# Kernel optimization log

Measured on AMD Instinct MI355X. Metric: run time of the kernel, lower is better.

The kernel has to match this reference:

```python
import jax, jax.numpy as jnp
import numpy as np

N, V, I, O, G = 16, 4096, 128, 128, 16


def setup_inputs() -> dict:
    key = jax.random.key(0)
    ks = jax.random.split(key, 7)
    stdv = 1.0 / np.sqrt(O)  # reset_parameters: uniform(-stdv, stdv)
    u = lambda k, shape: jax.random.uniform(k, shape, jnp.float32, -stdv, stdv)
    return {
        "x": jax.random.normal(ks[0], (N, V, I), jnp.float32),
        "hx": jax.random.normal(ks[1], (N, V, O), jnp.float32),
        "group_index": jax.random.randint(ks[2], (V,), 0, G),
        "weight_ih": u(ks[3], (3, G, O, I)),
        "bias_ih": u(ks[4], (3, G, O)),
        "weight_hh": u(ks[5], (3, G, O, O)),
        "bias_hh": u(ks[6], (3, G, O)),
    }


def reference(x, hx, group_index, weight_ih, bias_ih, weight_hh, bias_hh):
    # gather per-node weights: [3, V, O, I] / [3, V, O]
    w_ih = weight_ih[:, group_index]
    b_ih = bias_ih[:, group_index]
    w_hh = weight_hh[:, group_index]
    b_hh = bias_hh[:, group_index]

    def lin_x(xx, w, b):  # [N,V,I] x [V,O,I] -> [N,V,O]
        return jnp.einsum("nvi,voi->nvo", xx, w) + b[None]

    def lin_h(h, w, b):  # torch einsum 'NVO,VOO->NVO' takes diagonal of w
        wd = jnp.diagonal(w, axis1=-2, axis2=-1)  # [V,O]
        return h * wd[None] + b[None]

    r = jax.nn.sigmoid(lin_x(x, w_ih[0], b_ih[0]) + lin_h(hx, w_hh[0], b_hh[0]))
    z = jax.nn.sigmoid(lin_x(x, w_ih[1], b_ih[1]) + lin_h(hx, w_hh[1], b_hh[1]))
    n = jnp.tanh(lin_x(x, w_ih[2], b_ih[2]) + r * lin_h(hx, w_hh[2], b_hh[2]))
    return (1.0 - z) * n + z * hx
```

## Files before the change

kernel.cpp:

```cpp
#include <hip/hip_runtime.h>
#include <math.h>

#define NN 16
#define VV 4096
#define II 128
#define OO 128
#define GG 16

typedef __attribute__((ext_vector_type(8))) short bf16x8;
typedef __attribute__((ext_vector_type(4))) float f32x4;

__device__ inline unsigned short f2bf(float f) {
    union { float f; unsigned u; } c; c.f = f;
    unsigned r = c.u + 0x7FFFu + ((c.u >> 16) & 1u);
    return (unsigned short)(r >> 16);
}
__device__ inline float bf2f(unsigned short h) {
    union { unsigned u; float f; } c; c.u = ((unsigned)h) << 16;
    return c.f;
}
__device__ inline void split1(float f, unsigned short& hi, unsigned short& lo) {
    hi = f2bf(f);
    lo = f2bf(f - bf2f(hi));
}
__device__ inline bf16x8 as_bf(uint4 u) {
    union { uint4 u; bf16x8 b; } c; c.u = u; return c.b;
}
__device__ inline void pack8(const float4& a, const float4& b, uint4& ph, uint4& pl) {
    unsigned short hi[8], lo[8];
    split1(a.x, hi[0], lo[0]); split1(a.y, hi[1], lo[1]);
    split1(a.z, hi[2], lo[2]); split1(a.w, hi[3], lo[3]);
    split1(b.x, hi[4], lo[4]); split1(b.y, hi[5], lo[5]);
    split1(b.z, hi[6], lo[6]); split1(b.w, hi[7], lo[7]);
    ph.x = (unsigned)hi[0] | ((unsigned)hi[1] << 16);
    ph.y = (unsigned)hi[2] | ((unsigned)hi[3] << 16);
    ph.z = (unsigned)hi[4] | ((unsigned)hi[5] << 16);
    ph.w = (unsigned)hi[6] | ((unsigned)hi[7] << 16);
    pl.x = (unsigned)lo[0] | ((unsigned)lo[1] << 16);
    pl.y = (unsigned)lo[2] | ((unsigned)lo[3] << 16);
    pl.z = (unsigned)lo[4] | ((unsigned)lo[5] << 16);
    pl.w = (unsigned)lo[6] | ((unsigned)lo[7] << 16);
}

__global__ __launch_bounds__(256) void prepack_kernel(
    const float* __restrict__ w_ih, uint4* __restrict__ wp)
{
    const int t  = blockIdx.x * 256 + threadIdx.x;
    const int i8 = t & 15;
    const int o  = (t >> 4) & 127;
    const int gg = t >> 11;

    const float* src = w_ih + ((size_t)gg * OO + o) * II + i8 * 8;
    const float4 a = *(const float4*)src;
    const float4 b = *(const float4*)(src + 4);
    uint4 ph, pl;
    pack8(a, b, ph, pl);

    const int s    = i8 >> 2;
    const int kb   = i8 & 3;
    const int lane = kb * 16 + (o & 15);
    const int ct   = o >> 4;
    const int pidx = ((gg * 8 + ct) * 4 + s) * 64 + lane;
    wp[pidx * 2]     = ph;
    wp[pidx * 2 + 1] = pl;
}

template <bool PREPACKED>
__global__ __launch_bounds__(256, 4) void ggru_mfma_kernel(
    const float* __restrict__ x,
    const float* __restrict__ hx,
    const int*   __restrict__ gidx,
    const uint4* __restrict__ wp,
    const float* __restrict__ w_ih,
    const float* __restrict__ b_ih,
    const float* __restrict__ w_hh,
    const float* __restrict__ b_hh,
    float*       __restrict__ out)
{
    const int v    = blockIdx.x;
    const int tid  = threadIdx.x;
    const int lane = tid & 63;
    const int wv   = tid >> 6;
    const int g    = gidx[v];

    __shared__ uint4 xhS[256];
    __shared__ uint4 xlS[256];
    __shared__ float gbuf[3][NN][132];

    {
        const int row = tid >> 4;
        const int sk  = tid & 15;
        const int s   = sk >> 2, kb = sk & 3;
        const float* xp = x + ((size_t)row * VV + v) * II + s * 32 + kb * 8;
        const float4 xa = *(const float4*)xp;
        const float4 xb = *(const float4*)(xp + 4);
        uint4 ph, pl;
        pack8(xa, xb, ph, pl);
        xhS[s * 64 + kb * 16 + row] = ph;
        xlS[s * 64 + kb * 16 + row] = pl;
    }
    __syncthreads();

    int tb[6];
    const float* wraw[6];
    #pragma unroll
    for (int t = 0; t < 6; ++t) {
        const int col  = wv * 96 + t * 16;
        const int gate = col >> 7;
        const int ob   = col & 127;
        const int ct   = ob >> 4;
        tb[t] = ((gate * GG + g) * 8 + ct) * 4;
        wraw[t] = w_ih + (((size_t)gate * GG + g) * OO + ob + (lane & 15)) * II + (lane >> 4) * 8;
    }

    f32x4 acc[6];
    #pragma unroll
    for (int t = 0; t < 6; ++t) acc[t] = (f32x4){0.f, 0.f, 0.f, 0.f};

    #pragma unroll
    for (int s = 0; s < 4; ++s) {
        const bf16x8 ah = as_bf(xhS[s * 64 + lane]);
        const bf16x8 al = as_bf(xlS[s * 64 + lane]);
        #pragma unroll
        for (int t = 0; t < 6; ++t) {
            bf16x8 wh, wl;
            if (PREPACKED) {
                wh = as_bf(wp[(size_t)(tb[t] + s) * 128 + lane * 2]);
                wl = as_bf(wp[(size_t)(tb[t] + s) * 128 + lane * 2 + 1]);
            } else {
                const float4 wa = *(const float4*)(wraw[t] + s * 32);
                const float4 wb = *(const float4*)(wraw[t] + s * 32 + 4);
                uint4 ph, pl;
                pack8(wa, wb, ph, pl);
                wh = as_bf(ph);
                wl = as_bf(pl);
            }
            acc[t] = __builtin_amdgcn_mfma_f32_16x16x32_bf16(ah, wh, acc[t], 0, 0, 0);
            acc[t] = __builtin_amdgcn_mfma_f32_16x16x32_bf16(al, wh, acc[t], 0, 0, 0);
            acc[t] = __builtin_amdgcn_mfma_f32_16x16x32_bf16(ah, wl, acc[t], 0, 0, 0);
        }
    }

    #pragma unroll
    for (int t = 0; t < 6; ++t) {
        const int col  = wv * 96 + t * 16 + (lane & 15);
        const int gate = col >> 7;
        const int o    = col & 127;
        #pragma unroll
        for (int r = 0; r < 4; ++r) {
            gbuf[gate][(lane >> 4) * 4 + r][o] = acc[t][r];
        }
    }
    __syncthreads();

    {
        const int o  = tid & 127;
        const int rb = (tid >> 7) * 8;

        const float bi0 = b_ih[(0 * GG + g) * OO + o];
        const float bi1 = b_ih[(1 * GG + g) * OO + o];
        const float bi2 = b_ih[(2 * GG + g) * OO + o];
        const float bh0 = b_hh[(0 * GG + g) * OO + o];
        const float bh1 = b_hh[(1 * GG + g) * OO + o];
        const float bh2 = b_hh[(2 * GG + g) * OO + o];
        const float wd0 = w_hh[((size_t)(0 * GG + g) * OO + o) * OO + o];
        const float wd1 = w_hh[((size_t)(1 * GG + g) * OO + o) * OO + o];
        const float wd2 = w_hh[((size_t)(2 * GG + g) * OO + o) * OO + o];

        #pragma unroll
        for (int r = 0; r < 8; ++r) {
            const int row = rb + r;
            const size_t idx = ((size_t)row * VV + v) * OO + o;
            const float h = hx[idx];

            const float gr  = gbuf[0][row][o] + bi0 + fmaf(h, wd0, bh0);
            const float gz  = gbuf[1][row][o] + bi1 + fmaf(h, wd1, bh1);
            const float ghn = fmaf(h, wd2, bh2);

            const float rr = 1.f / (1.f + __expf(-gr));
            const float zz = 1.f / (1.f + __expf(-gz));

            float t = gbuf[2][row][o] + bi2 + rr * ghn;
            t = fminf(fmaxf(t, -15.f), 15.f);
            const float e2 = __expf(2.f * t);
            const float th = (e2 - 1.f) / (e2 + 1.f);

            out[idx] = (1.f - zz) * th + zz * h;
        }
    }
}

extern "C" void kernel_launch(void* const* d_in, const int* in_sizes, int n_in,
                              void* d_out, int out_size, void* d_ws, size_t ws_size,
                              hipStream_t stream) {
    const float* x    = (const float*)d_in[0];
    const float* hx   = (const float*)d_in[1];
    const int*   gidx = (const int*)d_in[2];
    const float* w_ih = (const float*)d_in[3];
    const float* b_ih = (const float*)d_in[4];
    const float* w_hh = (const float*)d_in[5];
    const float* b_hh = (const float*)d_in[6];
    float* out = (float*)d_out;
    uint4* wp  = (uint4*)d_ws;

    const size_t need = 98304ull * 32ull;
    if (ws_size >= need) {
        prepack_kernel<<<384, 256, 0, stream>>>(w_ih, wp);
        ggru_mfma_kernel<true><<<VV, 256, 0, stream>>>(
            x, hx, gidx, wp, w_ih, b_ih, w_hh, b_hh, out);
    } else {
        ggru_mfma_kernel<false><<<VV, 256, 0, stream>>>(
            x, hx, gidx, (const uint4*)nullptr, w_ih, b_ih, w_hh, b_hh, out);
    }
}
```

Measured before the change: 176.9 us.

## Assign all three gates per output column to one wave, skip LDS gate buffer

Each wave now computes the r, z and n gate accumulators for the same 32 output columns, so the GRU epilogue reads its inputs straight from MFMA accumulator registers. This removes the shared-memory gate buffer, its scattered stores and the second block barrier, and it shrinks the LDS footprint. Weight fragments for a k-step are now all loaded before the MFMAs that use them, which adds register pressure. The hx loads and output stores are now strided by lane group (16 consecutive columns per row), so they coalesce less well than the previous 128-wide row access.

Result: faster. 172.7 us (-2.4%).

```diff
diff --git a/kernel.cpp b/kernel.cpp
--- a/kernel.cpp
+++ b/kernel.cpp
@@ -85,7 +85,6 @@
 
     __shared__ uint4 xhS[256];
     __shared__ uint4 xlS[256];
-    __shared__ float gbuf[3][NN][132];
 
     {
         const int row = tid >> 4;
@@ -101,61 +100,72 @@
     }
     __syncthreads();
 
-    int tb[6];
-    const float* wraw[6];
-    #pragma unroll
-    for (int t = 0; t < 6; ++t) {
-        const int col  = wv * 96 + t * 16;
-        const int gate = col >> 7;
-        const int ob   = col & 127;
-        const int ct   = ob >> 4;
-        tb[t] = ((gate * GG + g) * 8 + ct) * 4;
-        wraw[t] = w_ih + (((size_t)gate * GG + g) * OO + ob + (lane & 15)) * II + (lane >> 4) * 8;
-    }
-
-    f32x4 acc[6];
-    #pragma unroll
-    for (int t = 0; t < 6; ++t) acc[t] = (f32x4){0.f, 0.f, 0.f, 0.f};
+    int tb[3][2];
+    const float* wraw[3][2];
+    #pragma unroll
+    for (int ga = 0; ga < 3; ++ga) {
+        #pragma unroll
+        for (int t = 0; t < 2; ++t) {
+            const int ct = wv * 2 + t;
+            tb[ga][t] = ((ga * GG + g) * 8 + ct) * 4;
+            wraw[ga][t] = w_ih + (((size_t)ga * GG + g) * OO + ct * 16 + (lane & 15)) * II
+                          + (lane >> 4) * 8;
+        }
+    }
+
+    f32x4 acc[3][2];
+    #pragma unroll
+    for (int ga = 0; ga < 3; ++ga)
+        #pragma unroll
+        for (int t = 0; t < 2; ++t)
+            acc[ga][t] = (f32x4){0.f, 0.f, 0.f, 0.f};
 
     #pragma unroll
     for (int s = 0; s < 4; ++s) {
         const bf16x8 ah = as_bf(xhS[s * 64 + lane]);
         const bf16x8 al = as_bf(xlS[s * 64 + lane]);
-        #pragma unroll
-        for (int t = 0; t < 6; ++t) {
-            bf16x8 wh, wl;
-            if (PREPACKED) {
-                wh = as_bf(wp[(size_t)(tb[t] + s) * 128 + lane * 2]);
-                wl = as_bf(wp[(size_t)(tb[t] + s) * 128 + lane * 2 + 1]);
-            } else {
-                const float4 wa = *(const float4*)(wraw[t] + s * 32);
-                const float4 wb = *(const float4*)(wraw[t] + s * 32 + 4);
-                uint4 ph, pl;
-                pack8(wa, wb, ph, pl);
-                wh = as_bf(ph);
-                wl = as_bf(pl);
+
+        uint4 wh6[6], wl6[6];
+        if (PREPACKED) {
+            #pragma unroll
+            for (int ga = 0; ga < 3; ++ga) {
+                #pragma unroll
+                for (int t = 0; t < 2; ++t) {
+                    const size_t base = (size_t)(tb[ga][t] + s) * 128 + lane * 2;
+                    wh6[ga * 2 + t] = wp[base];
+                    wl6[ga * 2 + t] = wp[base + 1];
+                }
             }
-            acc[t] = __builtin_amdgcn_mfma_f32_16x16x32_bf16(ah, wh, acc[t], 0, 0, 0);
-            acc[t] = __builtin_amdgcn_mfma_f32_16x16x32_bf16(al, wh, acc[t], 0, 0, 0);
-            acc[t] = __builtin_amdgcn_mfma_f32_16x16x32_bf16(ah, wl, acc[t], 0, 0, 0);
-        }
-    }
-
-    #pragma unroll
-    for (int t = 0; t < 6; ++t) {
-        const int col  = wv * 96 + t * 16 + (lane & 15);
-        const int gate = col >> 7;
-        const int o    = col & 127;
-        #pragma unroll
-        for (int r = 0; r < 4; ++r) {
-            gbuf[gate][(lane >> 4) * 4 + r][o] = acc[t][r];
-        }
-    }
-    __syncthreads();
-
-    {
-        const int o  = tid & 127;
-        const int rb = (tid >> 7) * 8;
+        } else {
+            #pragma unroll
+            for (int ga = 0; ga < 3; ++ga) {
+                #pragma unroll
+                for (int t = 0; t < 2; ++t) {
+                    const float4 wa = *(const float4*)(wraw[ga][t] + s * 32);
+                    const float4 wb = *(const float4*)(wraw[ga][t] + s * 32 + 4);
+                    pack8(wa, wb, wh6[ga * 2 + t], wl6[ga * 2 + t]);
+                }
+            }
+        }
+
+        #pragma unroll
+        for (int ga = 0; ga < 3; ++ga) {
+            #pragma unroll
+            for (int t = 0; t < 2; ++t) {
+                const bf16x8 wh = as_bf(wh6[ga * 2 + t]);
+                const bf16x8 wl = as_bf(wl6[ga * 2 + t]);
+                acc[ga][t] = __builtin_amdgcn_mfma_f32_16x16x32_bf16(ah, wh, acc[ga][t], 0, 0, 0);
+                acc[ga][t] = __builtin_amdgcn_mfma_f32_16x16x32_bf16(al, wh, acc[ga][t], 0, 0, 0);
+                acc[ga][t] = __builtin_amdgcn_mfma_f32_16x16x32_bf16(ah, wl, acc[ga][t], 0, 0, 0);
+            }
+        }
+    }
+
+    const int l15 = lane & 15;
+    const int rg  = lane >> 4;
+    #pragma unroll
+    for (int t = 0; t < 2; ++t) {
+        const int o = wv * 32 + t * 16 + l15;
 
         const float bi0 = b_ih[(0 * GG + g) * OO + o];
         const float bi1 = b_ih[(1 * GG + g) * OO + o];
@@ -168,21 +178,21 @@
         const float wd2 = w_hh[((size_t)(2 * GG + g) * OO + o) * OO + o];
 
         #pragma unroll
-        for (int r = 0; r < 8; ++r) {
-            const int row = rb + r;
+        for (int r = 0; r < 4; ++r) {
+            const int row = rg * 4 + r;
             const size_t idx = ((size_t)row * VV + v) * OO + o;
             const float h = hx[idx];
 
-            const float gr  = gbuf[0][row][o] + bi0 + fmaf(h, wd0, bh0);
-            const float gz  = gbuf[1][row][o] + bi1 + fmaf(h, wd1, bh1);
+            const float gr  = acc[0][t][r] + bi0 + fmaf(h, wd0, bh0);
+            const float gz  = acc[1][t][r] + bi1 + fmaf(h, wd1, bh1);
             const float ghn = fmaf(h, wd2, bh2);
 
             const float rr = 1.f / (1.f + __expf(-gr));
             const float zz = 1.f / (1.f + __expf(-gz));
 
-            float t = gbuf[2][row][o] + bi2 + rr * ghn;
-            t = fminf(fmaxf(t, -15.f), 15.f);
-            const float e2 = __expf(2.f * t);
+            float tt = acc[2][t][r] + bi2 + rr * ghn;
+            tt = fminf(fmaxf(tt, -15.f), 15.f);
+            const float e2 = __expf(2.f * tt);
             const float th = (e2 - 1.f) / (e2 + 1.f);
 
             out[idx] = (1.f - zz) * th + zz * h;
```
